# Kernel optimization log

Hardware: AMD Instinct MI355X
Metric: run time of the kernel (lower is better)

The kernel has to match this reference:

```python
import jax, jax.numpy as jnp
import numpy as np

EMBED_DIM = 1024
NUM_HEADS = 16
HEAD_DIM = EMBED_DIM // NUM_HEADS
BATCH = 2
SEQ = 2048


def setup_inputs() -> dict:
    key = jax.random.key(0)
    ks = jax.random.split(key, 9)
    scale = 1.0 / np.sqrt(EMBED_DIM)
    return {
        "inputs": jax.random.normal(ks[0], (BATCH, SEQ, EMBED_DIM), jnp.float32),
        "Wq": jax.random.normal(ks[1], (EMBED_DIM, EMBED_DIM), jnp.float32) * scale,
        "bq": jnp.zeros((EMBED_DIM,), jnp.float32),
        "Wk": jax.random.normal(ks[2], (EMBED_DIM, EMBED_DIM), jnp.float32) * scale,
        "bk": jnp.zeros((EMBED_DIM,), jnp.float32),
        "Wv": jax.random.normal(ks[3], (EMBED_DIM, EMBED_DIM), jnp.float32) * scale,
        "bv": jnp.zeros((EMBED_DIM,), jnp.float32),
        "Wo": jax.random.normal(ks[4], (EMBED_DIM, EMBED_DIM), jnp.float32) * scale,
        "bo": jnp.zeros((EMBED_DIM,), jnp.float32),
    }


def reference(inputs, Wq, bq, Wk, bk, Wv, bv, Wo, bo):
    B, S, D = inputs.shape
    H, Dh = NUM_HEADS, HEAD_DIM

    def split_heads(x):  # [B,S,D] -> [B,H,S,Dh]
        return x.reshape(B, S, H, Dh).transpose(0, 2, 1, 3)

    Q = split_heads(inputs @ Wq + bq)
    K = split_heads(inputs @ Wk + bk)
    V = split_heads(inputs @ Wv + bv)

    # naive full-score attention, faithful to the original
    scores = jnp.einsum("bhqd,bhkd->bhqk", Q, K) / jnp.sqrt(jnp.float32(Dh))
    weights = jax.nn.softmax(scores, axis=-1)
    out = jnp.einsum("bhqk,bhkd->bhqd", weights, V)

    concat = out.transpose(0, 2, 1, 3).reshape(B, S, D)
    return concat @ Wo + bo
```

## Files before the change

### kernel.cpp

```cpp
#include <hip/hip_runtime.h>

#define EMBED 1024
#define NHEAD 16
#define HDIM  64
#define BATCH 2
#define SEQ   2048
#define MTOK  (BATCH * SEQ)
#define QSCALE 0.1803368801f

typedef __bf16 bf16x8 __attribute__((ext_vector_type(8)));
typedef float  f32x4  __attribute__((ext_vector_type(4)));

__device__ __forceinline__ unsigned short f2bf(float f) {
  return (unsigned short)((__float_as_uint(f) + 0x8000u) >> 16);
}
__device__ __forceinline__ unsigned int pkbf(float a, float b) {
  unsigned int ua = __float_as_uint(a) + 0x8000u;
  unsigned int ub = __float_as_uint(b) + 0x8000u;
  return __builtin_amdgcn_perm(ub, ua, 0x07060302u);
}

__device__ __forceinline__ void gload_lds16(const unsigned short* g, unsigned short* l) {
  __builtin_amdgcn_global_load_lds((__attribute__((address_space(1))) void*)g,
                                   (__attribute__((address_space(3))) void*)l, 16, 0, 0);
}

__global__ __launch_bounds__(256)
void prep_k(const float* __restrict__ X, unsigned short* __restrict__ Xbf,
            const float* __restrict__ w0, const float* __restrict__ w1,
            const float* __restrict__ w2, const float* __restrict__ w3,
            unsigned short* __restrict__ t0, unsigned short* __restrict__ t1,
            unsigned short* __restrict__ t2, unsigned short* __restrict__ t3) {
  const int id = blockIdx.x;
  if (id < 4096) {
    int i = id * 256 + threadIdx.x;
    float4 f = reinterpret_cast<const float4*>(X)[i];
    reinterpret_cast<uint2*>(Xbf)[i] = make_uint2(pkbf(f.x, f.y), pkbf(f.z, f.w));
    return;
  }
  const int t = id - 4096;
  const float* s; unsigned short* d;
  switch (t >> 8) {
    case 0: s = w0; d = t0; break;
    case 1: s = w1; d = t1; break;
    case 2: s = w2; d = t2; break;
    default: s = w3; d = t3; break;
  }
  const int tt = t & 255;
  const int k0 = (tt >> 4) * 64, n0 = (tt & 15) * 64;
  __shared__ unsigned short T[64][65];
  for (int i = threadIdx.x; i < 4096; i += 256) {
    int r = i >> 6, c = i & 63;
    T[c][r] = f2bf(s[(size_t)(k0 + r) * EMBED + n0 + c]);
  }
  __syncthreads();
  for (int i = threadIdx.x; i < 4096; i += 256) {
    int r = i >> 6, c = i & 63;
    d[(size_t)(n0 + r) * EMBED + k0 + c] = T[r][c];
  }
}

template<int MODE, int BM>
__global__ void gemm_k(const unsigned short* __restrict__ A,
                       const unsigned short* __restrict__ Bt,
                       const float* __restrict__ b0, const float* __restrict__ b1,
                       const float* __restrict__ b2,
                       unsigned short* __restrict__ oQ, unsigned short* __restrict__ oK,
                       unsigned short* __restrict__ oV, float* __restrict__ oF) {
  constexpr int MI = BM / 32;
  constexpr int NT = EMBED / 32;
  constexpr int LPT = BM / 64 + 2;

  __shared__ unsigned short As[3][BM][32];
  __shared__ unsigned short Bs[3][128][32];

  const int tid = threadIdx.x, lane = tid & 63, wave = tid >> 6;
  const int lr = lane & 15, quad = lane >> 4;
  const int wm = (wave >> 1) * (BM / 2), wn = (wave & 1) * 64;
  const int row0 = blockIdx.x * BM, col0 = blockIdx.y * 128;
  const int srow = lane >> 2, sc = lane & 3;
  const int scsw = (sc ^ ((srow >> 1) & 3)) * 8;
  const int sw = (quad ^ ((lr >> 1) & 3)) * 8;

  const f32x4 fz = {0.f, 0.f, 0.f, 0.f};
  f32x4 acc[MI][4];
#pragma unroll
  for (int i = 0; i < MI; ++i)
#pragma unroll
    for (int j = 0; j < 4; ++j) acc[i][j] = fz;

  auto stage = [&](int bufi, int tt) {
#pragma unroll
    for (int g = 0; g < BM / 64; ++g) {
      int rbase = wave * (BM / 4) + g * 16;
      gload_lds16(&A[(size_t)(row0 + rbase + srow) * EMBED + tt * 32 + scsw],
                  &As[bufi][rbase][0]);
    }
#pragma unroll
    for (int g = 0; g < 2; ++g) {
      int rbase = wave * 32 + g * 16;
      gload_lds16(&Bt[(size_t)(col0 + rbase + srow) * EMBED + tt * 32 + scsw],
                  &Bs[bufi][rbase][0]);
    }
  };

  stage(0, 0);
  stage(1, 1);

  int buf = 0, sb = 2;
  for (int t = 0; t < NT; ++t) {
    if (t < NT - 1)
      asm volatile("s_waitcnt vmcnt(%0)" :: "n"(LPT) : "memory");
    else
      asm volatile("s_waitcnt vmcnt(0)" ::: "memory");
    __builtin_amdgcn_s_barrier();

    bf16x8 af[MI], bv[4];
#pragma unroll
    for (int i = 0; i < MI; ++i)
      af[i] = *reinterpret_cast<const bf16x8*>(&As[buf][wm + i * 16 + lr][sw]);
#pragma unroll
    for (int j = 0; j < 4; ++j)
      bv[j] = *reinterpret_cast<const bf16x8*>(&Bs[buf][wn + j * 16 + lr][sw]);

    __builtin_amdgcn_s_setprio(1);
#pragma unroll
    for (int i = 0; i < MI; ++i)
#pragma unroll
      for (int j = 0; j < 4; ++j)
        acc[i][j] = __builtin_amdgcn_mfma_f32_16x16x32_bf16(af[i], bv[j],
                                                            acc[i][j], 0, 0, 0);
    __builtin_amdgcn_s_setprio(0);

    if (t + 2 < NT) stage(sb, t + 2);
    buf = (buf == 2) ? 0 : buf + 1;
    sb  = (sb  == 2) ? 0 : sb  + 1;
  }

#pragma unroll
  for (int i = 0; i < MI; ++i) {
#pragma unroll
    for (int j = 0; j < 4; ++j) {
      const int col = col0 + wn + j * 16 + lr;
      if (MODE == 1) {
        const float bb = b0[col];
#pragma unroll
        for (int r = 0; r < 4; ++r) {
          const int row = row0 + wm + i * 16 + quad * 4 + r;
          oF[((size_t)row << 10) + col] = acc[i][j][r] + bb;
        }
      } else {
        const int which = col >> 10, cn = col & 1023;
        const float bb = (which == 0 ? b0 : which == 1 ? b1 : b2)[cn];
        const float sscale = (which == 0) ? QSCALE : 1.0f;
        const int h = cn >> 6, dd = cn & 63;
#pragma unroll
        for (int r = 0; r < 4; ++r) {
          const int row = row0 + wm + i * 16 + quad * 4 + r;
          const int b = row >> 11, ss = row & (SEQ - 1);
          const float v = (acc[i][j][r] + bb) * sscale;
          if (which == 0) {
            oQ[((((size_t)b * NHEAD + h) * SEQ + ss) << 6) + dd] = f2bf(v);
          } else if (which == 1) {
            oK[((((size_t)b * NHEAD + h) * SEQ + ss) << 6) + dd] = f2bf(v);
          } else {
            oV[(((size_t)b * NHEAD + h) * HDIM + dd) * SEQ + ss] = f2bf(v);
          }
        }
      }
    }
  }
}

__global__ __launch_bounds__(256, 2)
void attn_k(const unsigned short* __restrict__ Qb,
            const unsigned short* __restrict__ Kb,
            const unsigned short* __restrict__ Vt,
            unsigned short* __restrict__ Ctx) {
  __shared__ unsigned short QPs[128][64];
  __shared__ unsigned short Ks[2][64][64];
  __shared__ unsigned short Vs[2][64][64];
  const int tid = threadIdx.x, lane = tid & 63, wave = tid >> 6;
  const int lr = lane & 15, quad = lane >> 4;
  const int bh = blockIdx.x, qt = blockIdx.y;
  const size_t base = (size_t)bh * SEQ * HDIM;
  const int srow = lane >> 3, sc = lane & 7;
  const int sw0 = (quad ^ (lr & 7)) * 8;
  const int sw1 = ((quad ^ 4) ^ (lr & 7)) * 8;

#pragma unroll
  for (int g = 0; g < 4; ++g) {
    int rbase = wave * 32 + g * 8;
    int row = rbase + srow;
    gload_lds16(&Qb[base + (size_t)(qt * 128 + row) * HDIM + ((sc ^ (row & 7)) * 8)],
                &QPs[rbase][0]);
  }
#pragma unroll
  for (int g = 0; g < 2; ++g) {
    int rbase = wave * 16 + g * 8;
    int row = rbase + srow;
    gload_lds16(&Kb[base + (size_t)row * HDIM + ((sc ^ (row & 7)) * 8)],
                &Ks[0][rbase][0]);
    gload_lds16(&Vt[base + (size_t)row * SEQ + ((sc ^ (row & 7)) * 8)],
                &Vs[0][rbase][0]);
  }
  __syncthreads();

  bf16x8 qf[2][2];
#pragma unroll
  for (int g = 0; g < 2; ++g) {
    qf[g][0] = *reinterpret_cast<const bf16x8*>(&QPs[wave * 32 + g * 16 + lr][sw0]);
    qf[g][1] = *reinterpret_cast<const bf16x8*>(&QPs[wave * 32 + g * 16 + lr][sw1]);
  }
  __threadfence_block();

  float l_part[2] = {0.f, 0.f};
  const f32x4 fz = {0.f, 0.f, 0.f, 0.f};
  f32x4 oacc[2][4];
#pragma unroll
  for (int g = 0; g < 2; ++g)
#pragma unroll
    for (int d = 0; d < 4; ++d) oacc[g][d] = fz;

  constexpr int NT = SEQ / 64;
  for (int kt = 0;;) {
    const int buf = kt & 1;

    if (kt + 1 < NT) {
#pragma unroll
      for (int g = 0; g < 2; ++g) {
        int rbase = wave * 16 + g * 8;
        int row = rbase + srow;
        gload_lds16(&Kb[base + (size_t)((kt + 1) * 64 + row) * HDIM + ((sc ^ (row & 7)) * 8)],
                    &Ks[buf ^ 1][rbase][0]);
        gload_lds16(&Vt[base + (size_t)row * SEQ + (kt + 1) * 64 + ((sc ^ (row & 7)) * 8)],
                    &Vs[buf ^ 1][rbase][0]);
      }
    }

    f32x4 sc4[2][4];
#pragma unroll
    for (int nt = 0; nt < 4; ++nt) {
      bf16x8 kf0 = *reinterpret_cast<const bf16x8*>(&Ks[buf][nt * 16 + lr][sw0]);
      bf16x8 kf1 = *reinterpret_cast<const bf16x8*>(&Ks[buf][nt * 16 + lr][sw1]);
#pragma unroll
      for (int g = 0; g < 2; ++g) {
        f32x4 a = __builtin_amdgcn_mfma_f32_16x16x32_bf16(kf0, qf[g][0], fz, 0, 0, 0);
        sc4[g][nt] = __builtin_amdgcn_mfma_f32_16x16x32_bf16(kf1, qf[g][1], a, 0, 0, 0);
      }
    }

#pragma unroll
    for (int g = 0; g < 2; ++g)
#pragma unroll
      for (int nt = 0; nt < 4; ++nt) {
        float p0 = __builtin_amdgcn_exp2f(sc4[g][nt][0]);
        float p1 = __builtin_amdgcn_exp2f(sc4[g][nt][1]);
        float p2 = __builtin_amdgcn_exp2f(sc4[g][nt][2]);
        float p3 = __builtin_amdgcn_exp2f(sc4[g][nt][3]);
        l_part[g] += (p0 + p1) + (p2 + p3);
        const int pc = (nt * 2 + (quad >> 1)) ^ (lr & 7);
        *reinterpret_cast<uint2*>(&QPs[wave * 32 + g * 16 + lr][pc * 8 + (quad & 1) * 4]) =
            make_uint2(pkbf(p0, p1), pkbf(p2, p3));
      }

    __threadfence_block();

    bf16x8 pa[2][2];
#pragma unroll
    for (int g = 0; g < 2; ++g) {
      pa[g][0] = *reinterpret_cast<const bf16x8*>(&QPs[wave * 32 + g * 16 + lr][sw0]);
      pa[g][1] = *reinterpret_cast<const bf16x8*>(&QPs[wave * 32 + g * 16 + lr][sw1]);
    }
#pragma unroll
    for (int d = 0; d < 4; ++d) {
      bf16x8 vb0 = *reinterpret_cast<const bf16x8*>(&Vs[buf][d * 16 + lr][sw0]);
      bf16x8 vb1 = *reinterpret_cast<const bf16x8*>(&Vs[buf][d * 16 + lr][sw1]);
#pragma unroll
      for (int g = 0; g < 2; ++g) {
        oacc[g][d] = __builtin_amdgcn_mfma_f32_16x16x32_bf16(pa[g][0], vb0, oacc[g][d], 0, 0, 0);
        oacc[g][d] = __builtin_amdgcn_mfma_f32_16x16x32_bf16(pa[g][1], vb1, oacc[g][d], 0, 0, 0);
      }
    }

    if (++kt == NT) break;
    __syncthreads();
  }

#pragma unroll
  for (int g = 0; g < 2; ++g) {
    l_part[g] += __shfl_xor(l_part[g], 16);
    l_part[g] += __shfl_xor(l_part[g], 32);
  }

  const int b = bh >> 4, h = bh & 15;
#pragma unroll
  for (int g = 0; g < 2; ++g) {
    float linv[4];
#pragma unroll
    for (int r = 0; r < 4; ++r) linv[r] = 1.0f / __shfl(l_part[g], quad * 4 + r);
#pragma unroll
    for (int d = 0; d < 4; ++d)
#pragma unroll
      for (int r = 0; r < 4; ++r) {
        const int q = qt * 128 + wave * 32 + g * 16 + quad * 4 + r;
        Ctx[(((size_t)b * SEQ + q) << 10) + h * 64 + d * 16 + lr] =
            f2bf(oacc[g][d][r] * linv[r]);
      }
  }
}

extern "C" void kernel_launch(void* const* d_in, const int* in_sizes, int n_in,
                              void* d_out, int out_size, void* d_ws, size_t ws_size,
                              hipStream_t stream) {
  const float* X  = (const float*)d_in[0];
  const float* Wq = (const float*)d_in[1];
  const float* bq = (const float*)d_in[2];
  const float* Wk = (const float*)d_in[3];
  const float* bk = (const float*)d_in[4];
  const float* Wv = (const float*)d_in[5];
  const float* bv = (const float*)d_in[6];
  const float* Wo = (const float*)d_in[7];
  const float* bo = (const float*)d_in[8];

  unsigned short* ws = (unsigned short*)d_ws;
  const size_t M1 = (size_t)1024 * 1024;
  unsigned short* Xbf = ws;
  unsigned short* WqT = ws + 4 * M1;
  unsigned short* WkT = ws + 5 * M1;
  unsigned short* WvT = ws + 6 * M1;
  unsigned short* WoT = ws + 7 * M1;
  unsigned short* Qb  = ws + 8 * M1;
  unsigned short* Kb  = ws + 12 * M1;
  unsigned short* Vt  = ws + 16 * M1;
  unsigned short* Ctx = ws + 20 * M1;

  prep_k<<<5120, 256, 0, stream>>>(X, Xbf, Wq, Wk, Wv, Wo, WqT, WkT, WvT, WoT);

  gemm_k<0, 128><<<dim3(MTOK / 128, 3072 / 128), 256, 0, stream>>>(
      Xbf, WqT, bq, bk, bv, Qb, Kb, Vt, nullptr);

  attn_k<<<dim3(BATCH * NHEAD, SEQ / 128), 256, 0, stream>>>(Qb, Kb, Vt, Ctx);

  gemm_k<1, 64><<<dim3(MTOK / 64, EMBED / 128), 256, 0, stream>>>(
      Ctx, WoT, bo, nullptr, nullptr, nullptr, nullptr, nullptr, (float*)d_out);
}
```

Before: 189.1 us.

## Keep softmax probabilities in registers via permuted K row loading

K rows are loaded into shared memory in a permuted order, so each lane's score MFMA outputs already line up with the A-operand layout of the P·V MFMA. The exponentials are then packed straight into bf16x8 registers, removing the round trip of writing P to shared memory and reading it back, along with the associated fences. This cuts LDS traffic and latency in the attention inner loop, but it depends on the permutation exactly matching the MFMA register layout, or the results will be wrong.

```diff
diff --git a/kernel.cpp b/kernel.cpp
--- a/kernel.cpp
+++ b/kernel.cpp
@@ -23,6 +23,10 @@
 __device__ __forceinline__ void gload_lds16(const unsigned short* g, unsigned short* l) {
   __builtin_amdgcn_global_load_lds((__attribute__((address_space(1))) void*)g,
                                    (__attribute__((address_space(3))) void*)l, 16, 0, 0);
+}
+
+__device__ __forceinline__ int kperm(int r) {
+  return (r & 32) | (((r >> 2) & 3) << 3) | (((r >> 4) & 1) << 2) | (r & 3);
 }
 
 __global__ __launch_bounds__(256)
@@ -199,7 +203,7 @@
   for (int g = 0; g < 2; ++g) {
     int rbase = wave * 16 + g * 8;
     int row = rbase + srow;
-    gload_lds16(&Kb[base + (size_t)row * HDIM + ((sc ^ (row & 7)) * 8)],
+    gload_lds16(&Kb[base + (size_t)kperm(row) * HDIM + ((sc ^ (row & 7)) * 8)],
                 &Ks[0][rbase][0]);
     gload_lds16(&Vt[base + (size_t)row * SEQ + ((sc ^ (row & 7)) * 8)],
                 &Vs[0][rbase][0]);
@@ -212,7 +216,6 @@
     qf[g][0] = *reinterpret_cast<const bf16x8*>(&QPs[wave * 32 + g * 16 + lr][sw0]);
     qf[g][1] = *reinterpret_cast<const bf16x8*>(&QPs[wave * 32 + g * 16 + lr][sw1]);
   }
-  __threadfence_block();
 
   float l_part[2] = {0.f, 0.f};
   const f32x4 fz = {0.f, 0.f, 0.f, 0.f};
@@ -231,7 +234,7 @@
       for (int g = 0; g < 2; ++g) {
         int rbase = wave * 16 + g * 8;
         int row = rbase + srow;
-        gload_lds16(&Kb[base + (size_t)((kt + 1) * 64 + row) * HDIM + ((sc ^ (row & 7)) * 8)],
+        gload_lds16(&Kb[base + (size_t)((kt + 1) * 64 + kperm(row)) * HDIM + ((sc ^ (row & 7)) * 8)],
                     &Ks[buf ^ 1][rbase][0]);
         gload_lds16(&Vt[base + (size_t)row * SEQ + (kt + 1) * 64 + ((sc ^ (row & 7)) * 8)],
                     &Vs[buf ^ 1][rbase][0]);
@@ -250,36 +253,37 @@
       }
     }
 
+    bf16x8 pf[2][2];
 #pragma unroll
     for (int g = 0; g < 2; ++g)
 #pragma unroll
-      for (int nt = 0; nt < 4; ++nt) {
-        float p0 = __builtin_amdgcn_exp2f(sc4[g][nt][0]);
-        float p1 = __builtin_amdgcn_exp2f(sc4[g][nt][1]);
-        float p2 = __builtin_amdgcn_exp2f(sc4[g][nt][2]);
-        float p3 = __builtin_amdgcn_exp2f(sc4[g][nt][3]);
-        l_part[g] += (p0 + p1) + (p2 + p3);
-        const int pc = (nt * 2 + (quad >> 1)) ^ (lr & 7);
-        *reinterpret_cast<uint2*>(&QPs[wave * 32 + g * 16 + lr][pc * 8 + (quad & 1) * 4]) =
-            make_uint2(pkbf(p0, p1), pkbf(p2, p3));
-      }
-
-    __threadfence_block();
-
-    bf16x8 pa[2][2];
-#pragma unroll
-    for (int g = 0; g < 2; ++g) {
-      pa[g][0] = *reinterpret_cast<const bf16x8*>(&QPs[wave * 32 + g * 16 + lr][sw0]);
-      pa[g][1] = *reinterpret_cast<const bf16x8*>(&QPs[wave * 32 + g * 16 + lr][sw1]);
-    }
+      for (int b = 0; b < 2; ++b) {
+        float e0 = __builtin_amdgcn_exp2f(sc4[g][2 * b][0]);
+        float e1 = __builtin_amdgcn_exp2f(sc4[g][2 * b][1]);
+        float e2 = __builtin_amdgcn_exp2f(sc4[g][2 * b][2]);
+        float e3 = __builtin_amdgcn_exp2f(sc4[g][2 * b][3]);
+        l_part[g] += (e0 + e1) + (e2 + e3);
+        float o0 = __builtin_amdgcn_exp2f(sc4[g][2 * b + 1][0]);
+        float o1 = __builtin_amdgcn_exp2f(sc4[g][2 * b + 1][1]);
+        float o2 = __builtin_amdgcn_exp2f(sc4[g][2 * b + 1][2]);
+        float o3 = __builtin_amdgcn_exp2f(sc4[g][2 * b + 1][3]);
+        l_part[g] += (o0 + o1) + (o2 + o3);
+        union { unsigned int u[4]; bf16x8 v; } pk;
+        pk.u[0] = pkbf(e0, e1);
+        pk.u[1] = pkbf(e2, e3);
+        pk.u[2] = pkbf(o0, o1);
+        pk.u[3] = pkbf(o2, o3);
+        pf[g][b] = pk.v;
+      }
+
 #pragma unroll
     for (int d = 0; d < 4; ++d) {
       bf16x8 vb0 = *reinterpret_cast<const bf16x8*>(&Vs[buf][d * 16 + lr][sw0]);
       bf16x8 vb1 = *reinterpret_cast<const bf16x8*>(&Vs[buf][d * 16 + lr][sw1]);
 #pragma unroll
       for (int g = 0; g < 2; ++g) {
-        oacc[g][d] = __builtin_amdgcn_mfma_f32_16x16x32_bf16(pa[g][0], vb0, oacc[g][d], 0, 0, 0);
-        oacc[g][d] = __builtin_amdgcn_mfma_f32_16x16x32_bf16(pa[g][1], vb1, oacc[g][d], 0, 0, 0);
+        oacc[g][d] = __builtin_amdgcn_mfma_f32_16x16x32_bf16(pf[g][0], vb0, oacc[g][d], 0, 0, 0);
+        oacc[g][d] = __builtin_amdgcn_mfma_f32_16x16x32_bf16(pf[g][1], vb1, oacc[g][d], 0, 0, 0);
       }
     }
 
```

Measured after the change: 186.6 us. No clear change (-1.3%).
